# Kernel tuning notes

Hardware: AMD Instinct MI355X
Metric: run time of the kernel (lower is better)

## Reference

```python
import jax, jax.numpy as jnp
import numpy as np

EPS = 1e-6

def rmsnorm(x, w):
    var = jnp.mean(x * x, axis=-1, keepdims=True)
    return x * jax.lax.rsqrt(var + EPS) * w


def setup_inputs() -> dict:
    key = jax.random.key(0)
    ks = jax.random.split(key, 16)
    B, L, D = 1, 1024, 2048
    Di, N, K, R = 4096, 16, 4, 128
    I, E = 5632, 8
    s = 0.02
    inp = {}
    inp["hidden_states"] = jax.random.normal(ks[0], (B, L, D), jnp.float32)
    inp["ln_in_w"] = jnp.ones((D,), jnp.float32)
    inp["in_proj_w"] = jax.random.normal(ks[1], (2 * Di, D), jnp.float32) * s
    inp["conv_w"] = jax.random.normal(ks[2], (Di, K), jnp.float32) * 0.1
    inp["conv_b"] = jnp.zeros((Di,), jnp.float32)
    inp["x_proj_w"] = jax.random.normal(ks[3], (R + 2 * N, Di), jnp.float32) * s
    inp["dt_ln_w"] = jnp.ones((R,), jnp.float32)
    inp["b_ln_w"] = jnp.ones((N,), jnp.float32)
    inp["c_ln_w"] = jnp.ones((N,), jnp.float32)
    inp["dt_proj_w"] = jax.random.normal(ks[4], (Di, R), jnp.float32) * s
    inp["dt_proj_b"] = jax.random.uniform(ks[5], (Di,), jnp.float32, -4.0, -2.0)
    inp["A_log"] = jnp.log(jnp.broadcast_to(jnp.arange(1, N + 1, dtype=jnp.float32), (Di, N)))
    inp["D_param"] = jnp.ones((Di,), jnp.float32)
    inp["out_proj_w"] = jax.random.normal(ks[6], (D, Di), jnp.float32) * s
    inp["ln_ff_w"] = jnp.ones((D,), jnp.float32)
    inp["router_w"] = jax.random.normal(ks[7], (E, D), jnp.float32) * s
    inp["w1"] = jax.random.normal(ks[8], (E, I, D), jnp.float32) * s
    inp["w3"] = jax.random.normal(ks[9], (E, I, D), jnp.float32) * s
    inp["w2"] = jax.random.normal(ks[10], (E, D, I), jnp.float32) * s
    return inp


def reference(hidden_states, ln_in_w, in_proj_w, conv_w, conv_b, x_proj_w,
              dt_ln_w, b_ln_w, c_ln_w, dt_proj_w, dt_proj_b, A_log, D_param,
              out_proj_w, ln_ff_w, router_w, w1, w3, w2):
    Bb, L, D = hidden_states.shape
    Di = in_proj_w.shape[0] // 2
    N = b_ln_w.shape[0]
    R = dt_ln_w.shape[0]
    K = conv_w.shape[1]
    E = router_w.shape[0]
    TOP_K = 2

    # residual is None on layer entry: residual = x; hs = rmsnorm(x)
    residual = hidden_states
    hs = rmsnorm(hidden_states, ln_in_w)

    # ---- Mamba mixer ----
    xz = hs @ in_proj_w.T                          # [B,L,2Di]
    x, z = jnp.split(xz, 2, axis=-1)
    # causal depthwise conv1d (kernel K), pad left K-1
    xt = jnp.moveaxis(x, 1, 2)                     # [B,Di,L]
    xc = jax.lax.conv_general_dilated(
        xt, conv_w[:, None, :], (1,), [(K - 1, 0)],
        dimension_numbers=('NCH', 'OIH', 'NCH'), feature_group_count=Di)
    xc = jax.nn.silu(xc + conv_b[None, :, None])
    xc = jnp.moveaxis(xc, 1, 2)                    # [B,L,Di]

    xdb = xc @ x_proj_w.T                          # [B,L,R+2N]
    dt, Bm, Cm = jnp.split(xdb, [R, R + N], axis=-1)
    dt = rmsnorm(dt, dt_ln_w)
    Bm = rmsnorm(Bm, b_ln_w)
    Cm = rmsnorm(Cm, c_ln_w)
    dt = jax.nn.softplus(dt @ dt_proj_w.T + dt_proj_b)  # [B,L,Di]
    A = -jnp.exp(A_log)                            # [Di,N]

    def step(h, inps):
        dt_t, x_t, B_t, C_t = inps                 # [B,Di],[B,Di],[B,N],[B,N]
        dA = jnp.exp(dt_t[..., None] * A)          # [B,Di,N]
        h = h * dA + (dt_t * x_t)[..., None] * B_t[:, None, :]
        y = jnp.einsum('bdn,bn->bd', h, C_t)
        return h, y

    h0 = jnp.zeros((Bb, Di, N), hs.dtype)
    xs = (jnp.moveaxis(dt, 0, 1), jnp.moveaxis(xc, 0, 1),
          jnp.moveaxis(Bm, 0, 1), jnp.moveaxis(Cm, 0, 1))
    _, ys = jax.lax.scan(step, h0, xs)             # ys: [L,B,Di]
    y = jnp.moveaxis(ys, 0, 1)
    y = y + xc * D_param
    y = y * jax.nn.silu(z)
    mamba_out = y @ out_proj_w.T                   # [B,L,D]

    # ---- fused RMSNorm + residual ----
    residual = mamba_out + residual
    hs = rmsnorm(residual, ln_ff_w)

    # ---- MoE FFN (top-2, no renormalization) ----
    T = Bb * L
    flat = hs.reshape(T, D)
    logits = flat @ router_w.T                     # [T,E]
    probs = jax.nn.softmax(logits, axis=-1)
    topv, topi = jax.lax.top_k(probs, TOP_K)
    gate_w = jnp.sum(jax.nn.one_hot(topi, E, dtype=flat.dtype) * topv[..., None], axis=1)  # [T,E]
    g = jnp.einsum('td,eid->tei', flat, w1)
    u = jnp.einsum('td,eid->tei', flat, w3)
    yexp = jnp.einsum('tei,edi->ted', jax.nn.silu(g) * u, w2)
    moe_out = jnp.einsum('ted,te->td', yexp, gate_w).reshape(Bb, L, D)

    return moe_out, residual
```

## Files before the change

### kernel.cpp

```cpp
#include <hip/hip_runtime.h>
#include <hip/hip_bf16.h>
#include <stdint.h>

typedef __attribute__((ext_vector_type(4))) float f32x4;
typedef __attribute__((ext_vector_type(8))) short s16x8;
typedef __attribute__((ext_vector_type(8))) unsigned short u16x8;

#define LL 1024
#define DMODEL 2048
#define DI 4096
#define NSTATE 16
#define RDT 128
#define NEXP 8
#define IFF 5632

#define BM 128
#define BN 128
#define BK 32
#define G2CHUNK 2816
#define G2PARTS 2
#define MAXTILES 23

__device__ inline unsigned short f2bf(float f) {
  unsigned int u = __builtin_bit_cast(unsigned int, f);
  u += 0x7fffu + ((u >> 16) & 1u);
  return (unsigned short)(u >> 16);
}
__device__ inline unsigned short cvbf(float f) {
  return __builtin_bit_cast(unsigned short, __float2bfloat16(f));
}
__device__ inline float upbf(unsigned short h) {
  return __builtin_bit_cast(float, (unsigned int)h << 16);
}
__device__ inline float wred64(float v) {
#pragma unroll
  for (int m = 32; m; m >>= 1) v += __shfl_xor(v, m, 64);
  return v;
}
__device__ inline f32x4 mfma16(s16x8 a, s16x8 b, f32x4 c) {
  return __builtin_amdgcn_mfma_f32_16x16x32_bf16(a, b, c, 0, 0, 0);
}
__device__ inline int swz(int row, int chunk) {
  return row * 32 + (chunk ^ ((row & 3) << 3));
}
__device__ inline int swz64(int row, int chunk) {
  return row * 64 + (chunk ^ ((row & 7) << 3));
}
__device__ inline void cv8(f32x4 a, f32x4 b, u16x8& h) {
#pragma unroll
  for (int j = 0; j < 4; j++) { h[j] = cvbf(a[j]); h[4 + j] = cvbf(b[j]); }
}
__device__ inline void cv_split8(f32x4 a, f32x4 b, u16x8& h, u16x8& l) {
#pragma unroll
  for (int j = 0; j < 4; j++) {
    unsigned short hh = cvbf(a[j]); h[j] = hh; l[j] = cvbf(a[j] - upbf(hh));
    unsigned short hb = cvbf(b[j]); h[4 + j] = hb; l[4 + j] = cvbf(b[j] - upbf(hb));
  }
}
__device__ inline void pipe_sync() {
  __builtin_amdgcn_sched_barrier(0);
  asm volatile("s_waitcnt lgkmcnt(0)" ::: "memory");
  __builtin_amdgcn_sched_barrier(0);
  __builtin_amdgcn_s_barrier();
  __builtin_amdgcn_sched_barrier(0);
}

__global__ __launch_bounds__(256) void rmsnorm_k(
    const float* __restrict__ x, const float* __restrict__ w,
    const float* __restrict__ addin, float* __restrict__ resout,
    float* __restrict__ f32out, unsigned short* __restrict__ hiout,
    unsigned short* __restrict__ loout, unsigned short* __restrict__ bfout)
{
  int t = blockIdx.x, tid = threadIdx.x;
  size_t base = (size_t)t * DMODEL + tid * 8;
  f32x4 v0 = *(const f32x4*)(x + base);
  f32x4 v1 = *(const f32x4*)(x + base + 4);
  if (addin) {
    v0 += *(const f32x4*)(addin + base);
    v1 += *(const f32x4*)(addin + base + 4);
  }
  float ss = 0.f;
#pragma unroll
  for (int j = 0; j < 4; j++) ss += v0[j]*v0[j] + v1[j]*v1[j];
  ss = wred64(ss);
  __shared__ float sred[4];
  if ((tid & 63) == 0) sred[tid >> 6] = ss;
  __syncthreads();
  ss = sred[0] + sred[1] + sred[2] + sred[3];
  float sc = rsqrtf(ss * (1.f / DMODEL) + 1e-6f);
  if (resout) {
    *(f32x4*)(resout + base) = v0;
    *(f32x4*)(resout + base + 4) = v1;
  }
  f32x4 w0 = *(const f32x4*)(w + tid * 8);
  f32x4 w1 = *(const f32x4*)(w + tid * 8 + 4);
  f32x4 o0 = v0 * sc * w0, o1 = v1 * sc * w1;
  if (f32out) {
    *(f32x4*)(f32out + base) = o0;
    *(f32x4*)(f32out + base + 4) = o1;
  }
  if (hiout) {
    u16x8 h, l;
    cv_split8(o0, o1, h, l);
    *(u16x8*)(hiout + base) = h;
    *(u16x8*)(loout + base) = l;
  }
  if (bfout) {
    u16x8 ob;
#pragma unroll
    for (int j = 0; j < 4; j++) { ob[j] = f2bf(o0[j]); ob[4 + j] = f2bf(o1[j]); }
    *(u16x8*)(bfout + base) = ob;
  }
}

template<int EPI, int PS>
__global__ __launch_bounds__(256) void gemm_split_k(
    const float* __restrict__ A, const unsigned short* __restrict__ Ah,
    const unsigned short* __restrict__ Al, const float* __restrict__ W,
    float* __restrict__ C, int M, int N, int K, int kchunk,
    const float* __restrict__ bias)
{
  __shared__ unsigned short sA[2][2][128 * 32];
  __shared__ unsigned short sB[2][2][128 * 32];
  int tid = threadIdx.x;
  int n0 = blockIdx.x * BN, m0 = blockIdx.y * BM;
  int kbase = blockIdx.z * kchunk;
  C += (size_t)blockIdx.z * M * N;
  int lane = tid & 63, wave = tid >> 6;
  int wm = (wave >> 1) * 64, wn = (wave & 1) * 64;
  int lrow = lane & 15, lk = (lane >> 4) * 8;
  int ar = tid >> 1, ac = (tid & 1) * 16;
  int arow = m0 + ar; if (arow >= M) arow = M - 1;
  int wrow = n0 + ar; if (wrow >= N) wrow = N - 1;
  const float* aptr = A + (size_t)arow * K + kbase + ac;
  const unsigned short* ahp = Ah + (PS ? ((size_t)arow * K + kbase + ac) : 0);
  const unsigned short* alp = Al + (PS ? ((size_t)arow * K + kbase + ac) : 0);
  const float* wptr = W + (size_t)wrow * K + kbase + ac;
  const int NT = kchunk / BK;
  f32x4 ra0[4], ra1[4], rw0[4], rw1[4];
  u16x8 rah0[2], ral0[2], rah1[2], ral1[2];
  if constexpr (PS) {
    rah0[0] = *(const u16x8*)(ahp);      rah0[1] = *(const u16x8*)(ahp + 8);
    ral0[0] = *(const u16x8*)(alp);      ral0[1] = *(const u16x8*)(alp + 8);
    rah1[0] = *(const u16x8*)(ahp + BK); rah1[1] = *(const u16x8*)(ahp + BK + 8);
    ral1[0] = *(const u16x8*)(alp + BK); ral1[1] = *(const u16x8*)(alp + BK + 8);
  } else {
#pragma unroll
    for (int q = 0; q < 4; q++) {
      ra0[q] = *(const f32x4*)(aptr + 4 * q);
      ra1[q] = *(const f32x4*)(aptr + BK + 4 * q);
    }
  }
#pragma unroll
  for (int q = 0; q < 4; q++) {
    rw0[q] = *(const f32x4*)(wptr + 4 * q);
    rw1[q] = *(const f32x4*)(wptr + BK + 4 * q);
  }
  f32x4 acc[4][4] = {};
  int c0 = ac, c1 = ac + 8;

#define GS_STEP(PB, TT)                                                      \
  {                                                                          \
    if constexpr (PS) {                                                      \
      *(u16x8*)&sA[PB][0][swz(ar, c0)] = rah##PB[0];                         \
      *(u16x8*)&sA[PB][0][swz(ar, c1)] = rah##PB[1];                         \
      *(u16x8*)&sA[PB][1][swz(ar, c0)] = ral##PB[0];                         \
      *(u16x8*)&sA[PB][1][swz(ar, c1)] = ral##PB[1];                         \
    } else {                                                                 \
      u16x8 h0, l0, h1, l1;                                                  \
      cv_split8(ra##PB[0], ra##PB[1], h0, l0);                               \
      cv_split8(ra##PB[2], ra##PB[3], h1, l1);                               \
      *(u16x8*)&sA[PB][0][swz(ar, c0)] = h0;                                 \
      *(u16x8*)&sA[PB][1][swz(ar, c0)] = l0;                                 \
      *(u16x8*)&sA[PB][0][swz(ar, c1)] = h1;                                 \
      *(u16x8*)&sA[PB][1][swz(ar, c1)] = l1;                                 \
    }                                                                        \
    {                                                                        \
      u16x8 h0, l0, h1, l1;                                                  \
      cv_split8(rw##PB[0], rw##PB[1], h0, l0);                               \
      cv_split8(rw##PB[2], rw##PB[3], h1, l1);                               \
      *(u16x8*)&sB[PB][0][swz(ar, c0)] = h0;                                 \
      *(u16x8*)&sB[PB][1][swz(ar, c0)] = l0;                                 \
      *(u16x8*)&sB[PB][0][swz(ar, c1)] = h1;                                 \
      *(u16x8*)&sB[PB][1][swz(ar, c1)] = l1;                                 \
    }                                                                        \
    if ((TT) + 2 < NT) {                                                     \
      int kk = ((TT) + 2) * BK;                                              \
      if constexpr (PS) {                                                    \
        rah##PB[0] = *(const u16x8*)(ahp + kk);                              \
        rah##PB[1] = *(const u16x8*)(ahp + kk + 8);                          \
        ral##PB[0] = *(const u16x8*)(alp + kk);                              \
        ral##PB[1] = *(const u16x8*)(alp + kk + 8);                          \
      } else {                                                               \
        _Pragma("unroll")                                                    \
        for (int q = 0; q < 4; q++) ra##PB[q] = *(const f32x4*)(aptr + kk + 4 * q); \
      }                                                                      \
      _Pragma("unroll")                                                      \
      for (int q = 0; q < 4; q++) rw##PB[q] = *(const f32x4*)(wptr + kk + 4 * q); \
    }                                                                        \
    pipe_sync();                                                             \
    {                                                                        \
      s16x8 ah[4], al[4];                                                    \
      _Pragma("unroll")                                                      \
      for (int i = 0; i < 4; i++) {                                          \
        int r = wm + i * 16 + lrow;                                          \
        ah[i] = *(const s16x8*)&sA[PB][0][swz(r, lk)];                       \
        al[i] = *(const s16x8*)&sA[PB][1][swz(r, lk)];                       \
      }                                                                      \
      _Pragma("unroll")                                                      \
      for (int ni = 0; ni < 4; ni++) {                                       \
        int r = wn + ni * 16 + lrow;                                         \
        s16x8 bh = *(const s16x8*)&sB[PB][0][swz(r, lk)];                    \
        s16x8 bl = *(const s16x8*)&sB[PB][1][swz(r, lk)];                    \
        _Pragma("unroll")                                                    \
        for (int mi = 0; mi < 4; mi++) {                                     \
          f32x4 tc = acc[mi][ni];                                            \
          tc = mfma16(al[mi], bh, tc);                                       \
          tc = mfma16(ah[mi], bl, tc);                                       \
          tc = mfma16(ah[mi], bh, tc);                                       \
          acc[mi][ni] = tc;                                                  \
        }                                                                    \
      }                                                                      \
    }                                                                        \
  }

  for (int t = 0; t < NT; t += 2) { GS_STEP(0, t) GS_STEP(1, t + 1) }
#undef GS_STEP

  int rb = wm + (lane >> 4) * 4, cb = wn + (lane & 15);
#pragma unroll
  for (int mi = 0; mi < 4; mi++)
#pragma unroll
    for (int ni = 0; ni < 4; ni++) {
      int col = n0 + cb + ni * 16;
      if (col >= N) continue;
#pragma unroll
      for (int j = 0; j < 4; j++) {
        int row = m0 + rb + mi * 16 + j;
        if (row >= M) continue;
        float v = acc[mi][ni][j];
        if (EPI == 1) { v += bias[col]; v = (v > 20.f) ? v : log1pf(expf(v)); }
        C[(size_t)row * N + col] = v;
      }
    }
}

__global__ void reduce_parts_k(const float* __restrict__ src, float* __restrict__ dst,
                               int len, int parts)
{
  int i = (blockIdx.x * 256 + threadIdx.x) * 4;
  if (i >= len) return;
  f32x4 s = *(const f32x4*)(src + i);
  for (int p = 1; p < parts; p++) s += *(const f32x4*)(src + (size_t)p * len + i);
  *(f32x4*)(dst + i) = s;
}

__global__ __launch_bounds__(256) void conv_silu_k(
    const float* __restrict__ xz, const float* __restrict__ cw,
    const float* __restrict__ cb, float* __restrict__ xc)
{
  int idx = blockIdx.x * 256 + threadIdx.x;
  int t = idx >> 12, d = idx & (DI - 1);
  f32x4 w = *(const f32x4*)(cw + d * 4);
  float acc = cb[d];
#pragma unroll
  for (int k = 0; k < 4; k++) {
    int ts = t - 3 + k;
    if (ts >= 0) acc = fmaf(xz[(size_t)ts * 8192 + d], w[k], acc);
  }
  float v = acc / (1.f + __expf(-acc));
  xc[idx] = v;
}

__global__ void dtbc_norm_k(const float* __restrict__ xdb,
    const float* __restrict__ dtw, const float* __restrict__ bw, const float* __restrict__ cw,
    float* __restrict__ dtr, float* __restrict__ Bm, float* __restrict__ Cm)
{
  int t = blockIdx.x, lane = threadIdx.x;
  const float* row = xdb + (size_t)t * 160;
  float v1 = row[lane], v2 = row[64 + lane];
  float vb = (lane < 32) ? row[128 + lane] : 0.f;
  float sd = wred64(v1 * v1 + v2 * v2);
  float sb = wred64((lane < 16) ? vb * vb : 0.f);
  float sc = wred64((lane >= 16 && lane < 32) ? vb * vb : 0.f);
  float scd = rsqrtf(sd * (1.f / 128) + 1e-6f);
  dtr[(size_t)t * 128 + lane]      = v1 * scd * dtw[lane];
  dtr[(size_t)t * 128 + 64 + lane] = v2 * scd * dtw[64 + lane];
  if (lane < 16)      Bm[t * 16 + lane]      = vb * rsqrtf(sb * (1.f / 16) + 1e-6f) * bw[lane];
  else if (lane < 32) Cm[t * 16 + lane - 16] = vb * rsqrtf(sc * (1.f / 16) + 1e-6f) * cw[lane - 16];
}

__global__ __launch_bounds__(256) void scan_k(
    const float* __restrict__ dt, float* __restrict__ xcy,
    const float* __restrict__ xz, const float* __restrict__ Bm,
    const float* __restrict__ Cm, const float* __restrict__ A_log,
    const float* __restrict__ Dp)
{
  __shared__ float sdt[64][16], sxc[64][16], sz[64][16], sB[64][16], sC[64][16], sy[64][16];
  int tid = threadIdx.x;
  int dl = tid >> 4, n = tid & 15;
  int d0 = blockIdx.x * 16;
  int d = d0 + dl;
  float a = -__expf(A_log[d * 16 + n]);
  float dpar = Dp[d];
  float h = 0.f;
  for (int t0 = 0; t0 < LL; t0 += 64) {
#pragma unroll
    for (int i = 0; i < 4; i++) {
      int idx = i * 256 + tid;
      int tt = idx >> 4, c = idx & 15;
      int gt = t0 + tt;
      sdt[tt][c] = dt[(size_t)gt * DI + d0 + c];
      sxc[tt][c] = xcy[(size_t)gt * DI + d0 + c];
      sz[tt][c]  = xz[(size_t)gt * 8192 + DI + d0 + c];
      sB[tt][c]  = Bm[gt * 16 + c];
      sC[tt][c]  = Cm[gt * 16 + c];
    }
    __syncthreads();
    for (int tg = 0; tg < 64; tg += 8) {
      float yv[8];
#pragma unroll
      for (int u = 0; u < 8; u++) {
        int tt = tg + u;
        float dtv = sdt[tt][dl];
        float dA = __expf(dtv * a);
        h = h * dA + dtv * sxc[tt][dl] * sB[tt][n];
        yv[u] = h * sC[tt][n];
      }
#pragma unroll
      for (int u = 0; u < 8; u++) yv[u] += __shfl_xor(yv[u], 1, 64);
#pragma unroll
      for (int u = 0; u < 8; u++) yv[u] += __shfl_xor(yv[u], 2, 64);
#pragma unroll
      for (int u = 0; u < 8; u++) yv[u] += __shfl_xor(yv[u], 4, 64);
#pragma unroll
      for (int u = 0; u < 8; u++) yv[u] += __shfl_xor(yv[u], 8, 64);
      if (n == 0) {
#pragma unroll
        for (int u = 0; u < 8; u++) {
          int tt = tg + u;
          float xv = sxc[tt][dl], zv = sz[tt][dl];
          sy[tt][dl] = (yv[u] + xv * dpar) * (zv / (1.f + __expf(-zv)));
        }
      }
    }
    __syncthreads();
#pragma unroll
    for (int i = 0; i < 4; i++) {
      int idx = i * 256 + tid;
      int tt = idx >> 4, c = idx & 15;
      xcy[(size_t)(t0 + tt) * DI + d0 + c] = sy[tt][c];
    }
    __syncthreads();
  }
}

__global__ void router_topk_k(const float* __restrict__ hs2,
                              const float* __restrict__ rw,
                              int* __restrict__ topi, float* __restrict__ topv)
{
  int t = blockIdx.x, lane = threadIdx.x;
  float acc[NEXP] = {};
  const float* xr = hs2 + (size_t)t * DMODEL;
  for (int i = lane; i < DMODEL; i += 64) {
    float x = xr[i];
#pragma unroll
    for (int e = 0; e < NEXP; e++) acc[e] += x * rw[e * DMODEL + i];
  }
#pragma unroll
  for (int e = 0; e < NEXP; e++) acc[e] = wred64(acc[e]);
  if (lane == 0) {
    float mx = acc[0];
#pragma unroll
    for (int e = 1; e < NEXP; e++) mx = fmaxf(mx, acc[e]);
    float p[NEXP], s = 0.f;
#pragma unroll
    for (int e = 0; e < NEXP; e++) { p[e] = expf(acc[e] - mx); s += p[e]; }
    float inv = 1.f / s;
#pragma unroll
    for (int e = 0; e < NEXP; e++) p[e] *= inv;
    int i0 = 0;
#pragma unroll
    for (int e = 1; e < NEXP; e++) if (p[e] > p[i0]) i0 = e;
    int i1 = (i0 == 0) ? 1 : 0;
#pragma unroll
    for (int e = 0; e < NEXP; e++) if (e != i0 && p[e] > p[i1]) i1 = e;
    topi[2 * t] = i0; topi[2 * t + 1] = i1;
    topv[2 * t] = p[i0]; topv[2 * t + 1] = p[i1];
  }
}

__global__ void build_lists_k(const int* __restrict__ topi, const float* __restrict__ topv,
                              int* __restrict__ tok, float* __restrict__ gate,
                              int* __restrict__ slot, int* __restrict__ cnt,
                              int* __restrict__ offs, int* __restrict__ mt)
{
  int lane = threadIdx.x;
  int base[NEXP] = {};
  for (int t0 = 0; t0 < LL; t0 += 64) {
    int t = t0 + lane;
    int i0 = topi[2 * t], i1 = topi[2 * t + 1];
    float p0 = topv[2 * t], p1 = topv[2 * t + 1];
    unsigned long long below = (1ull << lane) - 1ull;
#pragma unroll
    for (int e = 0; e < NEXP; e++) {
      unsigned long long m0 = __ballot(i0 == e);
      if (i0 == e) {
        int pos = base[e] + __popcll(m0 & below);
        tok[e * LL + pos] = t; gate[e * LL + pos] = p0; slot[e * LL + pos] = 0;
      }
      base[e] += __popcll(m0);
      unsigned long long m1 = __ballot(i1 == e);
      if (i1 == e) {
        int pos = base[e] + __popcll(m1 & below);
        tok[e * LL + pos] = t; gate[e * LL + pos] = p1; slot[e * LL + pos] = 1;
      }
      base[e] += __popcll(m1);
    }
  }
  if (lane < NEXP) cnt[lane] = base[lane];
  if (lane == 0) {
    int o = 0;
#pragma unroll
    for (int e = 0; e < NEXP; e++) { offs[e] = o; o += base[e]; }
    int f = 0;
#pragma unroll
    for (int e = 0; e < NEXP; e++)
      for (int m0 = 0; m0 < base[e]; m0 += BM) {
        mt[1 + 2 * f] = e; mt[2 + 2 * f] = m0; f++;
      }
    mt[0] = f;
  }
}

__global__ __launch_bounds__(256, 2) void moe_gemm1_k(
    const unsigned short* __restrict__ hs2b,
    const float* __restrict__ w1, const float* __restrict__ w3,
    unsigned short* __restrict__ act,
    const int* __restrict__ tok, const int* __restrict__ cnt,
    const int* __restrict__ offs, const int* __restrict__ mt)
{
  int zt = blockIdx.z;
  if (zt >= mt[0]) return;
  int e  = mt[1 + 2 * zt];
  int m0 = mt[2 + 2 * zt];
  int ce = cnt[e];
  int n0 = blockIdx.x * 64;
  __shared__ unsigned short sA[2][128 * 64];
  __shared__ unsigned short sB1[2][64 * 64];
  __shared__ unsigned short sB2[2][64 * 64];
  const float* W1 = w1 + (size_t)e * IFF * DMODEL;
  const float* W3 = w3 + (size_t)e * IFF * DMODEL;
  int tid = threadIdx.x;
  int lane = tid & 63, wave = tid >> 6;
  int wm = (wave >> 1) * 64, wn = (wave & 1) * 32;
  int lrow = lane & 15, lk = (lane >> 4) * 8;
  int ar = tid >> 1, ac = (tid & 1) * 32;
  int br = tid >> 2, bc = (tid & 3) * 16;
  bool av = (m0 + ar) < ce;
  const unsigned short* aptr = hs2b + (size_t)(av ? tok[e * LL + m0 + ar] : 0) * DMODEL + ac;
  const float* w1p = W1 + (size_t)(n0 + br) * DMODEL + bc;
  const float* w3p = W3 + (size_t)(n0 + br) * DMODEL + bc;
  u16x8 ua0[4], ua1[4];
  f32x4 w1r0[4], w1r1[4], w3r0[4], w3r1[4];
#pragma unroll
  for (int q = 0; q < 4; q++) {
    ua0[q] = *(const u16x8*)(aptr + 8 * q);
    ua1[q] = *(const u16x8*)(aptr + 64 + 8 * q);
    w1r0[q] = *(const f32x4*)(w1p + 4 * q);
    w1r1[q] = *(const f32x4*)(w1p + 64 + 4 * q);
    w3r0[q] = *(const f32x4*)(w3p + 4 * q);
    w3r1[q] = *(const f32x4*)(w3p + 64 + 4 * q);
  }
  f32x4 acc1[4][2] = {}, acc2[4][2] = {};
  const int NT = DMODEL / 64;

#define G1_STEP(PB, TT)                                                      \
  {                                                                          \
    *(u16x8*)&sA[PB][swz64(ar, ac)]      = ua##PB[0];                        \
    *(u16x8*)&sA[PB][swz64(ar, ac + 8)]  = ua##PB[1];                        \
    *(u16x8*)&sA[PB][swz64(ar, ac + 16)] = ua##PB[2];                        \
    *(u16x8*)&sA[PB][swz64(ar, ac + 24)] = ua##PB[3];                        \
    u16x8 h;                                                                 \
    cv8(w1r##PB[0], w1r##PB[1], h); *(u16x8*)&sB1[PB][swz64(br, bc)]     = h;\
    cv8(w1r##PB[2], w1r##PB[3], h); *(u16x8*)&sB1[PB][swz64(br, bc + 8)] = h;\
    cv8(w3r##PB[0], w3r##PB[1], h); *(u16x8*)&sB2[PB][swz64(br, bc)]     = h;\
    cv8(w3r##PB[2], w3r##PB[3], h); *(u16x8*)&sB2[PB][swz64(br, bc + 8)] = h;\
    if ((TT) + 2 < NT) {                                                     \
      int kk = ((TT) + 2) * 64;                                              \
      _Pragma("unroll")                                                      \
      for (int q = 0; q < 4; q++) {                                          \
        ua##PB[q]  = *(const u16x8*)(aptr + kk + 8 * q);                     \
        w1r##PB[q] = *(const f32x4*)(w1p + kk + 4 * q);                      \
        w3r##PB[q] = *(const f32x4*)(w3p + kk + 4 * q);                      \
      }                                                                      \
    }                                                                        \
    pipe_sync();                                                             \
    _Pragma("unroll")                                                        \
    for (int ks = 0; ks < 2; ks++) {                                         \
      int ko = lk + ks * 32;                                                 \
      s16x8 af[4];                                                           \
      _Pragma("unroll")                                                      \
      for (int i = 0; i < 4; i++)                                            \
        af[i] = *(const s16x8*)&sA[PB][swz64(wm + i * 16 + lrow, ko)];       \
      _Pragma("unroll")                                                      \
      for (int ni = 0; ni < 2; ni++) {                                       \
        int r = wn + ni * 16 + lrow;                                         \
        s16x8 b1 = *(const s16x8*)&sB1[PB][swz64(r, ko)];                    \
        s16x8 b2 = *(const s16x8*)&sB2[PB][swz64(r, ko)];                    \
        _Pragma("unroll")                                                    \
        for (int mi = 0; mi < 4; mi++) acc1[mi][ni] = mfma16(af[mi], b1, acc1[mi][ni]); \
        _Pragma("unroll")                                                    \
        for (int mi = 0; mi < 4; mi++) acc2[mi][ni] = mfma16(af[mi], b2, acc2[mi][ni]); \
      }                                                                      \
    }                                                                        \
  }

  for (int t = 0; t < NT; t += 2) { G1_STEP(0, t) G1_STEP(1, t + 1) }
#undef G1_STEP

  int rb = wm + (lane >> 4) * 4, cb = wn + (lane & 15);
  int obase = offs[e];
#pragma unroll
  for (int mi = 0; mi < 4; mi++)
#pragma unroll
    for (int j = 0; j < 4; j++) {
      int row = m0 + rb + mi * 16 + j;
      if (row >= ce) continue;
#pragma unroll
      for (int ni = 0; ni < 2; ni++) {
        int col = n0 + cb + ni * 16;
        float g = acc1[mi][ni][j], u = acc2[mi][ni][j];
        float aval = (g / (1.f + __expf(-g))) * u;
        act[(size_t)(obase + row) * IFF + col] = f2bf(aval);
      }
    }
}

__global__ __launch_bounds__(256, 3) void moe_gemm2_k(
    const unsigned short* __restrict__ act, const float* __restrict__ w2,
    float* __restrict__ g2p,
    const int* __restrict__ tok, const float* __restrict__ gate,
    const int* __restrict__ slot, const int* __restrict__ cnt,
    const int* __restrict__ offs, const int* __restrict__ mt)
{
  int zt = blockIdx.z;
  if (zt >= mt[0]) return;
  int e  = mt[1 + 2 * zt];
  int m0 = mt[2 + 2 * zt];
  int ce = cnt[e];
  int part = blockIdx.y;
  int n0 = blockIdx.x * 64;
  int kbase = part * G2CHUNK;
  const int NT = G2CHUNK / 64;
  __shared__ unsigned short sA[2][128 * 64];
  __shared__ unsigned short sB[2][64 * 64];
  const float* W = w2 + (size_t)e * DMODEL * IFF;
  int obase = offs[e];
  int tid = threadIdx.x;
  int lane = tid & 63, wave = tid >> 6;
  int wm = (wave >> 1) * 64, wn = (wave & 1) * 32;
  int lrow = lane & 15, lk = (lane >> 4) * 8;
  int ar = tid >> 1, ac = (tid & 1) * 32;
  int br = tid >> 2, bc = (tid & 3) * 16;
  bool av = (m0 + ar) < ce;
  const unsigned short* aptr = act + (size_t)(obase + (av ? (m0 + ar) : 0)) * IFF + kbase + ac;
  const float* wp = W + (size_t)(n0 + br) * IFF + kbase + bc;
  u16x8 ua0[4], ua1[4];
  f32x4 rw0[4], rw1[4];
#pragma unroll
  for (int q = 0; q < 4; q++) {
    ua0[q] = *(const u16x8*)(aptr + 8 * q);
    ua1[q] = *(const u16x8*)(aptr + 64 + 8 * q);
    rw0[q] = *(const f32x4*)(wp + 4 * q);
    rw1[q] = *(const f32x4*)(wp + 64 + 4 * q);
  }
  f32x4 acc[4][2] = {};

#define G2_STEP(PB, TT)                                                      \
  {                                                                          \
    *(u16x8*)&sA[PB][swz64(ar, ac)]      = ua##PB[0];                        \
    *(u16x8*)&sA[PB][swz64(ar, ac + 8)]  = ua##PB[1];                        \
    *(u16x8*)&sA[PB][swz64(ar, ac + 16)] = ua##PB[2];                        \
    *(u16x8*)&sA[PB][swz64(ar, ac + 24)] = ua##PB[3];                        \
    u16x8 h;                                                                 \
    cv8(rw##PB[0], rw##PB[1], h); *(u16x8*)&sB[PB][swz64(br, bc)]     = h;   \
    cv8(rw##PB[2], rw##PB[3], h); *(u16x8*)&sB[PB][swz64(br, bc + 8)] = h;   \
    if ((TT) + 2 < NT) {                                                     \
      int kk = ((TT) + 2) * 64;                                              \
      _Pragma("unroll")                                                      \
      for (int q = 0; q < 4; q++) {                                          \
        ua##PB[q] = *(const u16x8*)(aptr + kk + 8 * q);                      \
        rw##PB[q] = *(const f32x4*)(wp + kk + 4 * q);                        \
      }                                                                      \
    }                                                                        \
    pipe_sync();                                                             \
    _Pragma("unroll")                                                        \
    for (int ks = 0; ks < 2; ks++) {                                         \
      int ko = lk + ks * 32;                                                 \
      s16x8 af[4];                                                           \
      _Pragma("unroll")                                                      \
      for (int i = 0; i < 4; i++)                                            \
        af[i] = *(const s16x8*)&sA[PB][swz64(wm + i * 16 + lrow, ko)];       \
      _Pragma("unroll")                                                      \
      for (int ni = 0; ni < 2; ni++) {                                       \
        s16x8 b = *(const s16x8*)&sB[PB][swz64(wn + ni * 16 + lrow, ko)];    \
        _Pragma("unroll")                                                    \
        for (int mi = 0; mi < 4; mi++) acc[mi][ni] = mfma16(af[mi], b, acc[mi][ni]); \
      }                                                                      \
    }                                                                        \
  }

  for (int t = 0; t < NT; t += 2) { G2_STEP(0, t) G2_STEP(1, t + 1) }
#undef G2_STEP

  int rb = wm + (lane >> 4) * 4, cb = wn + (lane & 15);
#pragma unroll
  for (int mi = 0; mi < 4; mi++)
#pragma unroll
    for (int j = 0; j < 4; j++) {
      int row = m0 + rb + mi * 16 + j;
      if (row >= ce) continue;
      int t = tok[e * LL + row];
      float g = gate[e * LL + row];
      int s = slot[e * LL + row];
      float* dst = g2p + ((size_t)(part * 2 + s) * LL + t) * DMODEL + n0 + cb;
#pragma unroll
      for (int ni = 0; ni < 2; ni++) dst[ni * 16] = acc[mi][ni][j] * g;
    }
}

__global__ void moe_combine_k(const float* __restrict__ ys, float* __restrict__ out) {
  size_t i = ((size_t)blockIdx.x * 256 + threadIdx.x) * 4;
  f32x4 s = *(const f32x4*)(ys + i);
#pragma unroll
  for (int p = 1; p < 2 * G2PARTS; p++)
    s += *(const f32x4*)(ys + (size_t)p * LL * DMODEL + i);
  *(f32x4*)(out + i) = s;
}

extern "C" void kernel_launch(void* const* d_in, const int* in_sizes, int n_in,
                              void* d_out, int out_size, void* d_ws, size_t ws_size,
                              hipStream_t stream)
{
  (void)in_sizes; (void)n_in; (void)out_size; (void)ws_size;
  const float* hidden     = (const float*)d_in[0];
  const float* ln_in_w    = (const float*)d_in[1];
  const float* in_proj_w  = (const float*)d_in[2];
  const float* conv_w     = (const float*)d_in[3];
  const float* conv_b     = (const float*)d_in[4];
  const float* x_proj_w   = (const float*)d_in[5];
  const float* dt_ln_w    = (const float*)d_in[6];
  const float* b_ln_w     = (const float*)d_in[7];
  const float* c_ln_w     = (const float*)d_in[8];
  const float* dt_proj_w  = (const float*)d_in[9];
  const float* dt_proj_b  = (const float*)d_in[10];
  const float* A_log      = (const float*)d_in[11];
  const float* D_param    = (const float*)d_in[12];
  const float* out_proj_w = (const float*)d_in[13];
  const float* ln_ff_w    = (const float*)d_in[14];
  const float* router_w   = (const float*)d_in[15];
  const float* w1         = (const float*)d_in[16];
  const float* w3         = (const float*)d_in[17];
  const float* w2         = (const float*)d_in[18];
  float* moe_out  = (float*)d_out;
  float* residual = (float*)d_out + (size_t)LL * DMODEL;

  char* p = (char*)d_ws;
  auto alloc = [&](size_t bytes) { char* r = p; p += (bytes + 255) & ~(size_t)255; return r; };
  unsigned short* hs_hi  = (unsigned short*)alloc((size_t)LL * DMODEL * 2);
  unsigned short* hs_lo  = (unsigned short*)alloc((size_t)LL * DMODEL * 2);
  float* xz              = (float*)alloc((size_t)LL * 2 * DI * 4);
  float* xc              = (float*)alloc((size_t)LL * DI * 4);
  float* xdb             = (float*)alloc((size_t)LL * 160 * 4);
  float* dtr             = (float*)alloc((size_t)LL * 128 * 4);
  float* Bm              = (float*)alloc((size_t)LL * 16 * 4);
  float* Cm              = (float*)alloc((size_t)LL * 16 * 4);
  float* dt_full         = (float*)alloc((size_t)LL * DI * 4);
  float* mamba_out       = (float*)alloc((size_t)LL * DMODEL * 4);
  float* hs2_f           = (float*)alloc((size_t)LL * DMODEL * 4);
  unsigned short* hs2_bf = (unsigned short*)alloc((size_t)LL * DMODEL * 2);
  int* topi              = (int*)alloc(LL * 2 * 4);
  float* topv            = (float*)alloc(LL * 2 * 4);
  int* tok               = (int*)alloc(NEXP * LL * 4);
  float* gate            = (float*)alloc(NEXP * LL * 4);
  int* slot              = (int*)alloc(NEXP * LL * 4);
  int* cnt               = (int*)alloc(256);
  int* offs              = (int*)alloc(256);
  int* mt                = (int*)alloc((1 + 2 * 64) * 4);
  float* xdb_parts        = dt_full;
  float* out_parts        = xz;
  unsigned short* act_buf = (unsigned short*)xz;
  float* g2parts          = (float*)((char*)act_buf + (size_t)2 * LL * IFF * 2);

  rmsnorm_k<<<LL, 256, 0, stream>>>(hidden, ln_in_w, nullptr, nullptr, nullptr, hs_hi, hs_lo, nullptr);
  gemm_split_k<0, 1><<<dim3(64, 8, 1), 256, 0, stream>>>(nullptr, hs_hi, hs_lo, in_proj_w, xz, LL, 2 * DI, DMODEL, DMODEL, nullptr);
  conv_silu_k<<<(LL * DI) / 256, 256, 0, stream>>>(xz, conv_w, conv_b, xc);
  gemm_split_k<0, 0><<<dim3(2, 8, 16), 256, 0, stream>>>(xc, nullptr, nullptr, x_proj_w, xdb_parts, LL, 160, DI, DI / 16, nullptr);
  reduce_parts_k<<<(LL * 160) / 1024, 256, 0, stream>>>(xdb_parts, xdb, LL * 160, 16);
  dtbc_norm_k<<<LL, 64, 0, stream>>>(xdb, dt_ln_w, b_ln_w, c_ln_w, dtr, Bm, Cm);
  gemm_split_k<1, 0><<<dim3(32, 8, 1), 256, 0, stream>>>(dtr, nullptr, nullptr, dt_proj_w, dt_full, LL, DI, RDT, RDT, dt_proj_b);
  scan_k<<<DI / 16, 256, 0, stream>>>(dt_full, xc, xz, Bm, Cm, A_log, D_param);
  gemm_split_k<0, 0><<<dim3(16, 8, 4), 256, 0, stream>>>(xc, nullptr, nullptr, out_proj_w, out_parts, LL, DMODEL, DI, DI / 4, nullptr);
  reduce_parts_k<<<(LL * DMODEL) / 1024, 256, 0, stream>>>(out_parts, mamba_out, LL * DMODEL, 4);
  rmsnorm_k<<<LL, 256, 0, stream>>>(mamba_out, ln_ff_w, hidden, residual, hs2_f, nullptr, nullptr, hs2_bf);
  router_topk_k<<<LL, 64, 0, stream>>>(hs2_f, router_w, topi, topv);
  build_lists_k<<<1, 64, 0, stream>>>(topi, topv, tok, gate, slot, cnt, offs, mt);
  moe_gemm1_k<<<dim3(88, 1, MAXTILES), 256, 0, stream>>>(hs2_bf, w1, w3, act_buf, tok, cnt, offs, mt);
  moe_gemm2_k<<<dim3(32, G2PARTS, MAXTILES), 256, 0, stream>>>(act_buf, w2, g2parts, tok, gate, slot, cnt, offs, mt);
  moe_combine_k<<<(LL * DMODEL) / (256 * 4), 256, 0, stream>>>(g2parts, moe_out);
}
```

Measured before the change: 905.6 us.

## Interleave global prefetch between MFMA halves with setprio; widen scan unroll

In both MoE GEMM kernels, the barrier now comes before the next-tile global loads, and those loads are placed between the two k-substeps of MFMA work. Each MFMA block is wrapped in s_setprio to raise wave priority. The goal is to overlap global load issue with matrix-core work and reduce stalls at the barrier. The selective-scan inner batch also grows from 8 to 16 timesteps to amortize the shuffle reductions, at the cost of more registers.

Result: no change. 906.2 us (median of 2 runs) (+0.1%).

```diff
diff --git a/kernel.cpp b/kernel.cpp
--- a/kernel.cpp
+++ b/kernel.cpp
@@ -317,10 +317,10 @@
       sC[tt][c]  = Cm[gt * 16 + c];
     }
     __syncthreads();
-    for (int tg = 0; tg < 64; tg += 8) {
-      float yv[8];
-#pragma unroll
-      for (int u = 0; u < 8; u++) {
+    for (int tg = 0; tg < 64; tg += 16) {
+      float yv[16];
+#pragma unroll
+      for (int u = 0; u < 16; u++) {
         int tt = tg + u;
         float dtv = sdt[tt][dl];
         float dA = __expf(dtv * a);
@@ -328,16 +328,16 @@
         yv[u] = h * sC[tt][n];
       }
 #pragma unroll
-      for (int u = 0; u < 8; u++) yv[u] += __shfl_xor(yv[u], 1, 64);
-#pragma unroll
-      for (int u = 0; u < 8; u++) yv[u] += __shfl_xor(yv[u], 2, 64);
-#pragma unroll
-      for (int u = 0; u < 8; u++) yv[u] += __shfl_xor(yv[u], 4, 64);
-#pragma unroll
-      for (int u = 0; u < 8; u++) yv[u] += __shfl_xor(yv[u], 8, 64);
+      for (int u = 0; u < 16; u++) yv[u] += __shfl_xor(yv[u], 1, 64);
+#pragma unroll
+      for (int u = 0; u < 16; u++) yv[u] += __shfl_xor(yv[u], 2, 64);
+#pragma unroll
+      for (int u = 0; u < 16; u++) yv[u] += __shfl_xor(yv[u], 4, 64);
+#pragma unroll
+      for (int u = 0; u < 16; u++) yv[u] += __shfl_xor(yv[u], 8, 64);
       if (n == 0) {
 #pragma unroll
-        for (int u = 0; u < 8; u++) {
+        for (int u = 0; u < 16; u++) {
           int tt = tg + u;
           float xv = sxc[tt][dl], zv = sz[tt][dl];
           sy[tt][dl] = (yv[u] + xv * dpar) * (zv / (1.f + __expf(-zv)));
@@ -475,6 +475,25 @@
   f32x4 acc1[4][2] = {}, acc2[4][2] = {};
   const int NT = DMODEL / 64;
 
+#define G1_MFMA(PB, KS)                                                      \
+    {                                                                        \
+      int ko = lk + (KS) * 32;                                               \
+      s16x8 af[4];                                                           \
+      _Pragma("unroll")                                                      \
+      for (int i = 0; i < 4; i++)                                            \
+        af[i] = *(const s16x8*)&sA[PB][swz64(wm + i * 16 + lrow, ko)];       \
+      _Pragma("unroll")                                                      \
+      for (int ni = 0; ni < 2; ni++) {                                       \
+        int r = wn + ni * 16 + lrow;                                         \
+        s16x8 b1 = *(const s16x8*)&sB1[PB][swz64(r, ko)];                    \
+        s16x8 b2 = *(const s16x8*)&sB2[PB][swz64(r, ko)];                    \
+        _Pragma("unroll")                                                    \
+        for (int mi = 0; mi < 4; mi++) acc1[mi][ni] = mfma16(af[mi], b1, acc1[mi][ni]); \
+        _Pragma("unroll")                                                    \
+        for (int mi = 0; mi < 4; mi++) acc2[mi][ni] = mfma16(af[mi], b2, acc2[mi][ni]); \
+      }                                                                      \
+    }
+
 #define G1_STEP(PB, TT)                                                      \
   {                                                                          \
     *(u16x8*)&sA[PB][swz64(ar, ac)]      = ua##PB[0];                        \
@@ -486,6 +505,10 @@
     cv8(w1r##PB[2], w1r##PB[3], h); *(u16x8*)&sB1[PB][swz64(br, bc + 8)] = h;\
     cv8(w3r##PB[0], w3r##PB[1], h); *(u16x8*)&sB2[PB][swz64(br, bc)]     = h;\
     cv8(w3r##PB[2], w3r##PB[3], h); *(u16x8*)&sB2[PB][swz64(br, bc + 8)] = h;\
+    pipe_sync();                                                             \
+    __builtin_amdgcn_s_setprio(1);                                           \
+    G1_MFMA(PB, 0)                                                           \
+    __builtin_amdgcn_s_setprio(0);                                           \
     if ((TT) + 2 < NT) {                                                     \
       int kk = ((TT) + 2) * 64;                                              \
       _Pragma("unroll")                                                      \
@@ -495,29 +518,14 @@
         w3r##PB[q] = *(const f32x4*)(w3p + kk + 4 * q);                      \
       }                                                                      \
     }                                                                        \
-    pipe_sync();                                                             \
-    _Pragma("unroll")                                                        \
-    for (int ks = 0; ks < 2; ks++) {                                         \
-      int ko = lk + ks * 32;                                                 \
-      s16x8 af[4];                                                           \
-      _Pragma("unroll")                                                      \
-      for (int i = 0; i < 4; i++)                                            \
-        af[i] = *(const s16x8*)&sA[PB][swz64(wm + i * 16 + lrow, ko)];       \
-      _Pragma("unroll")                                                      \
-      for (int ni = 0; ni < 2; ni++) {                                       \
-        int r = wn + ni * 16 + lrow;                                         \
-        s16x8 b1 = *(const s16x8*)&sB1[PB][swz64(r, ko)];                    \
-        s16x8 b2 = *(const s16x8*)&sB2[PB][swz64(r, ko)];                    \
-        _Pragma("unroll")                                                    \
-        for (int mi = 0; mi < 4; mi++) acc1[mi][ni] = mfma16(af[mi], b1, acc1[mi][ni]); \
-        _Pragma("unroll")                                                    \
-        for (int mi = 0; mi < 4; mi++) acc2[mi][ni] = mfma16(af[mi], b2, acc2[mi][ni]); \
-      }                                                                      \
-    }                                                                        \
+    __builtin_amdgcn_s_setprio(1);                                           \
+    G1_MFMA(PB, 1)                                                           \
+    __builtin_amdgcn_s_setprio(0);                                           \
   }
 
   for (int t = 0; t < NT; t += 2) { G1_STEP(0, t) G1_STEP(1, t + 1) }
 #undef G1_STEP
+#undef G1_MFMA
 
   int rb = wm + (lane >> 4) * 4, cb = wn + (lane & 15);
   int obase = offs[e];
@@ -577,6 +585,21 @@
   }
   f32x4 acc[4][2] = {};
 
+#define G2_MFMA(PB, KS)                                                      \
+    {                                                                        \
+      int ko = lk + (KS) * 32;                                               \
+      s16x8 af[4];                                                           \
+      _Pragma("unroll")                                                      \
+      for (int i = 0; i < 4; i++)                                            \
+        af[i] = *(const s16x8*)&sA[PB][swz64(wm + i * 16 + lrow, ko)];       \
+      _Pragma("unroll")                                                      \
+      for (int ni = 0; ni < 2; ni++) {                                       \
+        s16x8 b = *(const s16x8*)&sB[PB][swz64(wn + ni * 16 + lrow, ko)];    \
+        _Pragma("unroll")                                                    \
+        for (int mi = 0; mi < 4; mi++) acc[mi][ni] = mfma16(af[mi], b, acc[mi][ni]); \
+      }                                                                      \
+    }
+
 #define G2_STEP(PB, TT)                                                      \
   {                                                                          \
     *(u16x8*)&sA[PB][swz64(ar, ac)]      = ua##PB[0];                        \
@@ -586,6 +609,10 @@
     u16x8 h;                                                                 \
     cv8(rw##PB[0], rw##PB[1], h); *(u16x8*)&sB[PB][swz64(br, bc)]     = h;   \
     cv8(rw##PB[2], rw##PB[3], h); *(u16x8*)&sB[PB][swz64(br, bc + 8)] = h;   \
+    pipe_sync();                                                             \
+    __builtin_amdgcn_s_setprio(1);                                           \
+    G2_MFMA(PB, 0)                                                           \
+    __builtin_amdgcn_s_setprio(0);                                           \
     if ((TT) + 2 < NT) {                                                     \
       int kk = ((TT) + 2) * 64;                                              \
       _Pragma("unroll")                                                      \
@@ -594,25 +621,14 @@
         rw##PB[q] = *(const f32x4*)(wp + kk + 4 * q);                        \
       }                                                                      \
     }                                                                        \
-    pipe_sync();                                                             \
-    _Pragma("unroll")                                                        \
-    for (int ks = 0; ks < 2; ks++) {                                         \
-      int ko = lk + ks * 32;                                                 \
-      s16x8 af[4];                                                           \
-      _Pragma("unroll")                                                      \
-      for (int i = 0; i < 4; i++)                                            \
-        af[i] = *(const s16x8*)&sA[PB][swz64(wm + i * 16 + lrow, ko)];       \
-      _Pragma("unroll")                                                      \
-      for (int ni = 0; ni < 2; ni++) {                                       \
-        s16x8 b = *(const s16x8*)&sB[PB][swz64(wn + ni * 16 + lrow, ko)];    \
-        _Pragma("unroll")                                                    \
-        for (int mi = 0; mi < 4; mi++) acc[mi][ni] = mfma16(af[mi], b, acc[mi][ni]); \
-      }                                                                      \
-    }                                                                        \
+    __builtin_amdgcn_s_setprio(1);                                           \
+    G2_MFMA(PB, 1)                                                           \
+    __builtin_amdgcn_s_setprio(0);                                           \
   }
 
   for (int t = 0; t < NT; t += 2) { G2_STEP(0, t) G2_STEP(1, t + 1) }
 #undef G2_STEP
+#undef G2_MFMA
 
   int rb = wm + (lane >> 4) * 4, cb = wn + (lane & 15);
 #pragma unroll
```
